# Performance work log

Measured on AMD Instinct MI355X. Metric: run time of the kernel, lower is better.

The kernel has to match this reference:

```python
import jax, jax.numpy as jnp
import numpy as np

INPUT_DIM, K, L, D_C = 512, 3, 512, 64
LN_EPS = 1e-5
NORM_EPS = 1e-12


def setup_inputs() -> dict:
    key = jax.random.key(0)
    ks = jax.random.split(key, 16)
    s = 0.02
    inp = {
        "x": jax.random.normal(ks[0], (65536, INPUT_DIM), jnp.float32),
        # per-sub-encoder MLP weights, stacked over K
        "W1": jax.random.normal(ks[1], (K, INPUT_DIM, 256), jnp.float32) * s,
        "b1": jnp.zeros((K, 256), jnp.float32),
        "W2": jax.random.normal(ks[2], (K, 256, 128), jnp.float32) * s,
        "b2": jnp.zeros((K, 128), jnp.float32),
        "W3": jax.random.normal(ks[3], (K, 128, D_C), jnp.float32) * s,
        "b3": jnp.zeros((K, D_C), jnp.float32),
        # shared output LayerNorm
        "gamma": jnp.ones((D_C,), jnp.float32),
        "beta": jnp.zeros((D_C,), jnp.float32),
        # codebooks: nn.Parameter(torch.randn(L, d_c)) per sub-quantizer
        "codebooks": jax.random.normal(ks[4], (K, L, D_C), jnp.float32),
        # decoder MLP d_c -> 128 -> 256 -> input_dim
        "D1": jax.random.normal(ks[5], (D_C, 128), jnp.float32) * s,
        "c1": jnp.zeros((128,), jnp.float32),
        "D2": jax.random.normal(ks[6], (128, 256), jnp.float32) * s,
        "c2": jnp.zeros((256,), jnp.float32),
        "D3": jax.random.normal(ks[7], (256, INPUT_DIM), jnp.float32) * s,
        "c3": jnp.zeros((INPUT_DIM,), jnp.float32),
    }
    return inp


def _l2norm(v, axis=-1):
    # F.normalize(p=2): x / max(||x||, eps)
    n = jnp.sqrt(jnp.sum(v * v, axis=axis, keepdims=True))
    return v / jnp.maximum(n, NORM_EPS)


def reference(x, W1, b1, W2, b2, W3, b3, gamma, beta, codebooks,
              D1, c1, D2, c2, D3, c3):
    sg = jax.lax.stop_gradient
    # encode all K sub-encoders in one batched einsum: (K, B, *)
    h = jax.nn.relu(jnp.einsum('bi,kio->kbo', x, W1) + b1[:, None, :])
    h = jax.nn.relu(jnp.einsum('kbo,kop->kbp', h, W2) + b2[:, None, :])
    enc = jnp.einsum('kbp,kpd->kbd', h, W3) + b3[:, None, :]  # (K,B,d_c)
    # LayerNorm over d_c
    mu = jnp.mean(enc, axis=-1, keepdims=True)
    var = jnp.mean((enc - mu) ** 2, axis=-1, keepdims=True)
    enc = (enc - mu) * jax.lax.rsqrt(var + LN_EPS) * gamma + beta
    # cosine quantize
    enc_n = _l2norm(enc)
    cb_n = _l2norm(codebooks)                       # (K,L,d_c)
    cos = jnp.einsum('kbd,kld->kbl', enc_n, cb_n)   # (K,B,L)
    idx = jnp.argmax(cos, axis=-1)                  # argmin(1-cos) == argmax(cos), (K,B)
    q = jnp.take_along_axis(cb_n, idx[:, :, None], axis=1)  # (K,B,d_c)
    # straight-through
    q_ste = enc + sg(q - enc)
    codebook_loss = jnp.sum(jnp.mean((sg(enc) - q_ste) ** 2, axis=(1, 2)))
    commitment_loss = jnp.sum(jnp.mean((enc - sg(q_ste)) ** 2, axis=(1, 2)))
    avg_q = jnp.mean(q_ste, axis=0)                 # (B,d_c)
    h = jax.nn.relu(avg_q @ D1 + c1)
    h = jax.nn.relu(h @ D2 + c2)
    reconstructed = h @ D3 + c3                     # (B,input_dim)
    recon_loss = jnp.mean((reconstructed - x) ** 2)
    tokens = idx.T                                  # (B,K)
    return tokens, reconstructed, recon_loss, codebook_loss, commitment_loss
```

## Files before the change

### kernel.cpp

```cpp
#include <hip/hip_runtime.h>

using f4 = float4;

constexpr int IN_DIM = 512;
constexpr int DC     = 64;
constexpr int LCB    = 512;

__device__ __forceinline__ float wave_sum64(float v) {
#pragma unroll
    for (int m = 1; m < 64; m <<= 1) v += __shfl_xor(v, m, 64);
    return v;
}

__global__ void cbnorm_kernel(const float* __restrict__ cb, float* __restrict__ cbn,
                              float* __restrict__ cbnT, float* __restrict__ accv) {
    int row  = blockIdx.x * 4 + (threadIdx.x >> 6);
    int lane = threadIdx.x & 63;
    float v  = cb[(size_t)row * DC + lane];
    float ss = wave_sum64(v * v);
    float n  = sqrtf(ss);
    float o  = v / fmaxf(n, 1e-12f);
    cbn[(size_t)row * DC + lane] = o;
    int k = row >> 9, l = row & 511;
    cbnT[((size_t)k * DC + lane) * LCB + l] = o;
    if (blockIdx.x == 0 && threadIdx.x < 16) accv[threadIdx.x] = 0.f;
}

template <int RELU, int SUM3>
__global__ __launch_bounds__(256, 4)
void gemm_kernel(const float* __restrict__ A, const float* __restrict__ W,
                 const float* __restrict__ bias, float* __restrict__ C,
                 int Kin, int N, float ascale,
                 size_t aK, size_t wK, size_t bK, size_t cK, size_t sumStride) {
    constexpr int BM = 128, BK = 32;
    __shared__ alignas(16) float As[BK][BM + 4];
    __shared__ alignas(16) float Ws[BK][128 + 4];
    const int z = blockIdx.z;
    A += (size_t)z * aK;  W += (size_t)z * wK;
    bias += (size_t)z * bK;  C += (size_t)z * cK;
    const int tid = threadIdx.x;
    const int tx = tid & 15, ty = tid >> 4;
    const int row0 = blockIdx.x * BM, col0 = blockIdx.y * 128;

    float acc[8][8];
#pragma unroll
    for (int i = 0; i < 8; i++)
#pragma unroll
        for (int j = 0; j < 8; j++) acc[i][j] = 0.f;

    const int aRow = tid >> 3;
    const int aCol = (tid & 7) * 4;
    const int wRow = tid >> 5;
    const int wCol = (tid & 31) * 4;

    for (int kk = 0; kk < Kin; kk += BK) {
#pragma unroll
        for (int it = 0; it < 4; it++) {
            const size_t aoff = (size_t)(row0 + aRow + it * 32) * Kin + kk + aCol;
            f4 v = *(const f4*)&A[aoff];
            if (SUM3) {
                f4 v2 = *(const f4*)&A[aoff + sumStride];
                f4 v3 = *(const f4*)&A[aoff + 2 * sumStride];
                v.x += v2.x + v3.x; v.y += v2.y + v3.y;
                v.z += v2.z + v3.z; v.w += v2.w + v3.w;
            }
            As[aCol + 0][aRow + it * 32] = v.x * ascale;
            As[aCol + 1][aRow + it * 32] = v.y * ascale;
            As[aCol + 2][aRow + it * 32] = v.z * ascale;
            As[aCol + 3][aRow + it * 32] = v.w * ascale;
        }
#pragma unroll
        for (int it = 0; it < 4; it++) {
            f4 v = *(const f4*)&W[(size_t)(kk + wRow + it * 8) * N + col0 + wCol];
            *(f4*)&Ws[wRow + it * 8][wCol] = v;
        }
        __syncthreads();
#pragma unroll
        for (int p = 0; p < BK; p++) {
            f4 a0 = *(const f4*)&As[p][ty * 8];
            f4 a1 = *(const f4*)&As[p][ty * 8 + 4];
            f4 w0 = *(const f4*)&Ws[p][tx * 8];
            f4 w1 = *(const f4*)&Ws[p][tx * 8 + 4];
            float av[8] = {a0.x, a0.y, a0.z, a0.w, a1.x, a1.y, a1.z, a1.w};
            float wv[8] = {w0.x, w0.y, w0.z, w0.w, w1.x, w1.y, w1.z, w1.w};
#pragma unroll
            for (int i = 0; i < 8; i++)
#pragma unroll
                for (int j = 0; j < 8; j++)
                    acc[i][j] = fmaf(av[i], wv[j], acc[i][j]);
        }
        __syncthreads();
    }

#pragma unroll
    for (int i = 0; i < 8; i++) {
        const size_t r = (size_t)row0 + ty * 8 + i;
        float vrow[8];
#pragma unroll
        for (int j = 0; j < 8; j++) {
            float v = acc[i][j] + bias[col0 + tx * 8 + j];
            if (RELU) v = fmaxf(v, 0.f);
            vrow[j] = v;
        }
        *(f4*)&C[r * N + col0 + tx * 8]     = *(f4*)&vrow[0];
        *(f4*)&C[r * N + col0 + tx * 8 + 4] = *(f4*)&vrow[4];
    }
}

__global__ __launch_bounds__(256, 4)
void gemm_ln_kernel(const float* __restrict__ A, const float* __restrict__ W,
                    const float* __restrict__ bias, const float* __restrict__ gamma,
                    const float* __restrict__ beta, float* __restrict__ enc, int Kin,
                    size_t aK, size_t wK, size_t bK, size_t eK) {
    constexpr int BM = 128, BK = 32;
    __shared__ alignas(16) float As[BK][BM + 4];
    __shared__ alignas(16) float Ws[BK][DC + 4];
    const int z = blockIdx.y;
    A += (size_t)z * aK;  W += (size_t)z * wK;
    bias += (size_t)z * bK;  enc += (size_t)z * eK;
    const int tid = threadIdx.x;
    const int tx = tid & 7, ty = tid >> 3;
    const int row0 = blockIdx.x * BM;

    float acc[4][8];
#pragma unroll
    for (int i = 0; i < 4; i++)
#pragma unroll
        for (int j = 0; j < 8; j++) acc[i][j] = 0.f;

    const int aRow = tid >> 3;
    const int aCol = (tid & 7) * 4;
    const int wRow = tid >> 4;
    const int wCol = (tid & 15) * 4;

    for (int kk = 0; kk < Kin; kk += BK) {
#pragma unroll
        for (int it = 0; it < 4; it++) {
            f4 v = *(const f4*)&A[(size_t)(row0 + aRow + it * 32) * Kin + kk + aCol];
            As[aCol + 0][aRow + it * 32] = v.x;
            As[aCol + 1][aRow + it * 32] = v.y;
            As[aCol + 2][aRow + it * 32] = v.z;
            As[aCol + 3][aRow + it * 32] = v.w;
        }
#pragma unroll
        for (int it = 0; it < 2; it++) {
            f4 v = *(const f4*)&W[(size_t)(kk + wRow + it * 16) * DC + wCol];
            *(f4*)&Ws[wRow + it * 16][wCol] = v;
        }
        __syncthreads();
#pragma unroll
        for (int p = 0; p < BK; p++) {
            f4 a  = *(const f4*)&As[p][ty * 4];
            f4 w0 = *(const f4*)&Ws[p][tx * 8];
            f4 w1 = *(const f4*)&Ws[p][tx * 8 + 4];
            float av[4] = {a.x, a.y, a.z, a.w};
            float wv[8] = {w0.x, w0.y, w0.z, w0.w, w1.x, w1.y, w1.z, w1.w};
#pragma unroll
            for (int i = 0; i < 4; i++)
#pragma unroll
                for (int j = 0; j < 8; j++)
                    acc[i][j] = fmaf(av[i], wv[j], acc[i][j]);
        }
        __syncthreads();
    }

#pragma unroll
    for (int i = 0; i < 4; i++) {
        float vrow[8];
#pragma unroll
        for (int j = 0; j < 8; j++) vrow[j] = acc[i][j] + bias[tx * 8 + j];
        float s = 0.f;
#pragma unroll
        for (int j = 0; j < 8; j++) s += vrow[j];
#pragma unroll
        for (int m = 1; m < 8; m <<= 1) s += __shfl_xor(s, m, 8);
        float mu = s * (1.f / 64.f);
        float d2 = 0.f;
#pragma unroll
        for (int j = 0; j < 8; j++) { float d = vrow[j] - mu; d2 = fmaf(d, d, d2); }
#pragma unroll
        for (int m = 1; m < 8; m <<= 1) d2 += __shfl_xor(d2, m, 8);
        float rs = 1.f / sqrtf(d2 * (1.f / 64.f) + 1e-5f);
#pragma unroll
        for (int j = 0; j < 8; j++) {
            int c = tx * 8 + j;
            vrow[j] = (vrow[j] - mu) * rs * gamma[c] + beta[c];
        }
        const size_t r = (size_t)row0 + ty * 4 + i;
        *(f4*)&enc[r * DC + tx * 8]     = *(f4*)&vrow[0];
        *(f4*)&enc[r * DC + tx * 8 + 4] = *(f4*)&vrow[4];
    }
}

__global__ __launch_bounds__(256, 2)
void quant_kernel(float* __restrict__ enc, const float* __restrict__ cbT,
                  const float* __restrict__ cbn, float* __restrict__ out_tok,
                  float* __restrict__ sse_acc, int row_off_glob,
                  size_t eK, size_t cbTK, size_t cbnK) {
    constexpr int BM = 128;
    __shared__ alignas(16) float Es[DC][BM + 4];
    __shared__ alignas(16) float Cs[DC][64 + 4];
    __shared__ float red[4];
    const int k = blockIdx.y;
    enc += (size_t)k * eK;
    cbT += (size_t)k * cbTK;
    cbn += (size_t)k * cbnK;
    const int tid = threadIdx.x;
    const int tx = tid & 7, ty = tid >> 3;
    const int row0 = blockIdx.x * BM;

    {
        const int r  = tid >> 1;
        const int c0 = (tid & 1) * 32;
#pragma unroll
        for (int i = 0; i < 8; i++) {
            f4 v = *(const f4*)&enc[(size_t)(row0 + r) * DC + c0 + i * 4];
            Es[c0 + i * 4 + 0][r] = v.x;
            Es[c0 + i * 4 + 1][r] = v.y;
            Es[c0 + i * 4 + 2][r] = v.z;
            Es[c0 + i * 4 + 3][r] = v.w;
        }
    }

    double mx[4]; int mi[4];
#pragma unroll
    for (int i = 0; i < 4; i++) { mx[i] = -1.0e300; mi[i] = 0; }

    for (int lc = 0; lc < LCB; lc += 64) {
        __syncthreads();
        {
            const int p  = tid >> 2;
            const int c0 = (tid & 3) * 16;
#pragma unroll
            for (int i = 0; i < 4; i++)
                *(f4*)&Cs[p][c0 + i * 4] =
                    *(const f4*)&cbT[(size_t)p * LCB + lc + c0 + i * 4];
        }
        __syncthreads();
        double sc[4][8];
#pragma unroll
        for (int i = 0; i < 4; i++)
#pragma unroll
            for (int j = 0; j < 8; j++) sc[i][j] = 0.0;
#pragma unroll
        for (int p = 0; p < DC; p++) {
            f4 a  = *(const f4*)&Es[p][ty * 4];
            f4 w0 = *(const f4*)&Cs[p][tx * 8];
            f4 w1 = *(const f4*)&Cs[p][tx * 8 + 4];
            double av[4] = {a.x, a.y, a.z, a.w};
            double wv[8] = {w0.x, w0.y, w0.z, w0.w, w1.x, w1.y, w1.z, w1.w};
#pragma unroll
            for (int i = 0; i < 4; i++)
#pragma unroll
                for (int j = 0; j < 8; j++)
                    sc[i][j] = fma(av[i], wv[j], sc[i][j]);
        }
#pragma unroll
        for (int i = 0; i < 4; i++)
#pragma unroll
            for (int j = 0; j < 8; j++) {
                int l = lc + tx * 8 + j;
                if (sc[i][j] > mx[i]) { mx[i] = sc[i][j]; mi[i] = l; }
            }
    }

#pragma unroll
    for (int m = 1; m < 8; m <<= 1)
#pragma unroll
        for (int i = 0; i < 4; i++) {
            double omx = __shfl_xor(mx[i], m, 8);
            int    omi = __shfl_xor(mi[i], m, 8);
            if (omx > mx[i] || (omx == mx[i] && omi < mi[i])) { mx[i] = omx; mi[i] = omi; }
        }

    float sse = 0.f;
#pragma unroll
    for (int i = 0; i < 4; i++) {
        const int rl = ty * 4 + i;
        const size_t r = (size_t)row0 + rl;
        f4 q0 = *(const f4*)&cbn[(size_t)mi[i] * DC + tx * 8];
        f4 q1 = *(const f4*)&cbn[(size_t)mi[i] * DC + tx * 8 + 4];
        float qv[8] = {q0.x, q0.y, q0.z, q0.w, q1.x, q1.y, q1.z, q1.w};
#pragma unroll
        for (int j = 0; j < 8; j++) {
            float e = Es[tx * 8 + j][rl];
            float d = e - qv[j];
            sse = fmaf(d, d, sse);
        }
        *(f4*)&enc[r * DC + tx * 8]     = q0;
        *(f4*)&enc[r * DC + tx * 8 + 4] = q1;
        if (tx == 0) out_tok[(size_t)(row_off_glob + r) * 3 + k] = (float)mi[i];
    }
    sse = wave_sum64(sse);
    if ((tid & 63) == 0) red[tid >> 6] = sse;
    __syncthreads();
    if (tid == 0) atomicAdd(sse_acc, red[0] + red[1] + red[2] + red[3]);
}

__global__ __launch_bounds__(256, 4)
void gemm_dec_out_kernel(const float* __restrict__ A, const float* __restrict__ W,
                         const float* __restrict__ bias, const float* __restrict__ x,
                         float* __restrict__ rec, float* __restrict__ sse_acc,
                         int Kin, int N) {
    constexpr int BM = 128, BN = 128, BK = 32;
    __shared__ alignas(16) float As[BK][BM + 4];
    __shared__ alignas(16) float Ws[BK][BN + 4];
    __shared__ float red[4];
    const int tid = threadIdx.x;
    const int tx = tid & 15, ty = tid >> 4;
    const int row0 = blockIdx.x * BM, col0 = blockIdx.y * BN;

    float acc[8][8];
#pragma unroll
    for (int i = 0; i < 8; i++)
#pragma unroll
        for (int j = 0; j < 8; j++) acc[i][j] = 0.f;

    const int aRow = tid >> 3;
    const int aCol = (tid & 7) * 4;
    const int wRow = tid >> 5;
    const int wCol = (tid & 31) * 4;

    for (int kk = 0; kk < Kin; kk += BK) {
#pragma unroll
        for (int it = 0; it < 4; it++) {
            f4 v = *(const f4*)&A[(size_t)(row0 + aRow + it * 32) * Kin + kk + aCol];
            As[aCol + 0][aRow + it * 32] = v.x;
            As[aCol + 1][aRow + it * 32] = v.y;
            As[aCol + 2][aRow + it * 32] = v.z;
            As[aCol + 3][aRow + it * 32] = v.w;
        }
#pragma unroll
        for (int it = 0; it < 4; it++) {
            f4 v = *(const f4*)&W[(size_t)(kk + wRow + it * 8) * N + col0 + wCol];
            *(f4*)&Ws[wRow + it * 8][wCol] = v;
        }
        __syncthreads();
#pragma unroll
        for (int p = 0; p < BK; p++) {
            f4 a0 = *(const f4*)&As[p][ty * 8];
            f4 a1 = *(const f4*)&As[p][ty * 8 + 4];
            f4 w0 = *(const f4*)&Ws[p][tx * 8];
            f4 w1 = *(const f4*)&Ws[p][tx * 8 + 4];
            float av[8] = {a0.x, a0.y, a0.z, a0.w, a1.x, a1.y, a1.z, a1.w};
            float wv[8] = {w0.x, w0.y, w0.z, w0.w, w1.x, w1.y, w1.z, w1.w};
#pragma unroll
            for (int i = 0; i < 8; i++)
#pragma unroll
                for (int j = 0; j < 8; j++)
                    acc[i][j] = fmaf(av[i], wv[j], acc[i][j]);
        }
        __syncthreads();
    }

    float sse = 0.f;
#pragma unroll
    for (int i = 0; i < 8; i++) {
        const size_t r = (size_t)row0 + ty * 8 + i;
        f4 x0 = *(const f4*)&x[r * N + col0 + tx * 8];
        f4 x1 = *(const f4*)&x[r * N + col0 + tx * 8 + 4];
        float xv[8] = {x0.x, x0.y, x0.z, x0.w, x1.x, x1.y, x1.z, x1.w};
        float vrow[8];
#pragma unroll
        for (int j = 0; j < 8; j++) {
            float v = acc[i][j] + bias[col0 + tx * 8 + j];
            float d = v - xv[j];
            sse = fmaf(d, d, sse);
            vrow[j] = v;
        }
        *(f4*)&rec[r * N + col0 + tx * 8]     = *(f4*)&vrow[0];
        *(f4*)&rec[r * N + col0 + tx * 8 + 4] = *(f4*)&vrow[4];
    }
    sse = wave_sum64(sse);
    if ((tid & 63) == 0) red[tid >> 6] = sse;
    __syncthreads();
    if (tid == 0) atomicAdd(sse_acc, red[0] + red[1] + red[2] + red[3]);
}

__global__ void finalize_kernel(const float* __restrict__ accv,
                                float* __restrict__ outs,
                                float inv_rec, float inv_cb) {
    if (threadIdx.x == 0) {
        outs[0] = accv[1] * inv_rec;
        float cbl = accv[0] * inv_cb;
        outs[1] = cbl;
        outs[2] = cbl;
    }
}

extern "C" void kernel_launch(void* const* d_in, const int* in_sizes, int n_in,
                              void* d_out, int out_size, void* d_ws, size_t ws_size,
                              hipStream_t stream) {
    const float* x     = (const float*)d_in[0];
    const float* W1    = (const float*)d_in[1];
    const float* b1    = (const float*)d_in[2];
    const float* W2    = (const float*)d_in[3];
    const float* b2    = (const float*)d_in[4];
    const float* W3    = (const float*)d_in[5];
    const float* b3    = (const float*)d_in[6];
    const float* gamma = (const float*)d_in[7];
    const float* beta  = (const float*)d_in[8];
    const float* cb    = (const float*)d_in[9];
    const float* D1    = (const float*)d_in[10];
    const float* c1    = (const float*)d_in[11];
    const float* D2    = (const float*)d_in[12];
    const float* c2    = (const float*)d_in[13];
    const float* D3    = (const float*)d_in[14];
    const float* c3    = (const float*)d_in[15];
    const int M = in_sizes[0] / IN_DIM;

    float* out     = (float*)d_out;
    float* out_tok = out;
    float* out_rec = out + (size_t)M * 3;
    float* out_sc  = out_rec + (size_t)M * IN_DIM;

    const size_t fixedB  = (size_t)(16 + 2 * 3 * LCB * DC) * 4;
    const size_t perRowB = (size_t)(3 * DC + 3 * 256 + 3 * 128) * 4;
    int C = 4096;
    for (int cand = 65536; cand >= 4096; cand >>= 1)
        if (fixedB + (size_t)cand * perRowB <= ws_size) { C = cand; break; }

    float* ws    = (float*)d_ws;
    float* accv  = ws;
    float* cbn   = accv + 16;
    float* cbnT  = cbn + 3 * LCB * DC;
    float* enc3  = cbnT + 3 * DC * LCB;
    float* H1    = enc3 + (size_t)3 * C * DC;
    float* H2    = H1 + (size_t)3 * C * 256;

    cbnorm_kernel<<<dim3(3 * LCB / 4), dim3(256), 0, stream>>>(cb, cbn, cbnT, accv);

    for (int off = 0; off < M; off += C) {
        const float* xc  = x + (size_t)off * IN_DIM;
        float*       rcc = out_rec + (size_t)off * IN_DIM;

        gemm_kernel<1, 0><<<dim3(C / 128, 2, 3), dim3(256), 0, stream>>>(
            xc, W1, b1, H1, 512, 256, 1.f,
            0, (size_t)512 * 256, 256, (size_t)C * 256, 0);
        gemm_kernel<1, 0><<<dim3(C / 128, 1, 3), dim3(256), 0, stream>>>(
            H1, W2, b2, H2, 256, 128, 1.f,
            (size_t)C * 256, (size_t)256 * 128, 128, (size_t)C * 128, 0);
        gemm_ln_kernel<<<dim3(C / 128, 3), dim3(256), 0, stream>>>(
            H2, W3, b3, gamma, beta, enc3, 128,
            (size_t)C * 128, (size_t)128 * 64, 64, (size_t)C * DC);
        quant_kernel<<<dim3(C / 128, 3), dim3(256), 0, stream>>>(
            enc3, cbnT, cbn, out_tok, accv + 0, off,
            (size_t)C * DC, (size_t)DC * LCB, (size_t)LCB * DC);

        gemm_kernel<1, 1><<<dim3(C / 128, 1, 1), dim3(256), 0, stream>>>(
            enc3, D1, c1, H2, 64, 128, 1.f / 3.f,
            0, 0, 0, 0, (size_t)C * DC);
        gemm_kernel<1, 0><<<dim3(C / 128, 2, 1), dim3(256), 0, stream>>>(
            H2, D2, c2, H1, 128, 256, 1.f, 0, 0, 0, 0, 0);
        gemm_dec_out_kernel<<<dim3(C / 128, 4), dim3(256), 0, stream>>>(
            H1, D3, c3, xc, rcc, accv + 1, 256, 512);
    }

    finalize_kernel<<<dim3(1), dim3(64), 0, stream>>>(
        accv, out_sc, 1.f / ((float)M * IN_DIM), 1.f / ((float)M * DC));
}
```

Measured before the change: 1.374 ms.

## Register-prefetch next K tile in GEMMs and remap LDS layout to cut conflicts

The three tiled GEMM kernels (generic, LN-fused, decoder-output) now load the next K-slice of A and W into registers while the current slice is being computed from shared memory. This overlaps global-memory latency with FMA work, and the loop is rearranged to use a sync before and after the shared-memory store. The transposed A tile padding changes from +4 to +1, which targets bank conflicts on the scattered stores. The W tile drops its padding, and each thread's columns are remapped to tx*4 and 64+tx*4 so shared-memory reads are contiguous across threads, with the epilogue indexing adjusted to match. The +1 row stride makes the float4 reads of As misaligned on odd rows, which may force split or slower LDS accesses, and the extra live registers may reduce occupancy.

```diff
diff --git a/kernel.cpp b/kernel.cpp
--- a/kernel.cpp
+++ b/kernel.cpp
@@ -32,15 +32,15 @@
                  const float* __restrict__ bias, float* __restrict__ C,
                  int Kin, int N, float ascale,
                  size_t aK, size_t wK, size_t bK, size_t cK, size_t sumStride) {
-    constexpr int BM = 128, BK = 32;
-    __shared__ alignas(16) float As[BK][BM + 4];
-    __shared__ alignas(16) float Ws[BK][128 + 4];
+    constexpr int BM = 128, BN = 128, BK = 32;
+    __shared__ alignas(16) float As[BK][BM + 1];
+    __shared__ alignas(16) float Ws[BK][BN];
     const int z = blockIdx.z;
     A += (size_t)z * aK;  W += (size_t)z * wK;
     bias += (size_t)z * bK;  C += (size_t)z * cK;
     const int tid = threadIdx.x;
     const int tx = tid & 15, ty = tid >> 4;
-    const int row0 = blockIdx.x * BM, col0 = blockIdx.y * 128;
+    const int row0 = blockIdx.x * BM, col0 = blockIdx.y * BN;
 
     float acc[8][8];
 #pragma unroll
@@ -53,34 +53,52 @@
     const int wRow = tid >> 5;
     const int wCol = (tid & 31) * 4;
 
+    f4 ra[4], rw[4];
+#pragma unroll
+    for (int it = 0; it < 4; it++) {
+        const size_t aoff = (size_t)(row0 + aRow + it * 32) * Kin + aCol;
+        ra[it] = *(const f4*)&A[aoff];
+        if (SUM3) {
+            f4 v2 = *(const f4*)&A[aoff + sumStride];
+            f4 v3 = *(const f4*)&A[aoff + 2 * sumStride];
+            ra[it].x += v2.x + v3.x; ra[it].y += v2.y + v3.y;
+            ra[it].z += v2.z + v3.z; ra[it].w += v2.w + v3.w;
+        }
+        rw[it] = *(const f4*)&W[(size_t)(wRow + it * 8) * N + col0 + wCol];
+    }
+
     for (int kk = 0; kk < Kin; kk += BK) {
+        __syncthreads();
 #pragma unroll
         for (int it = 0; it < 4; it++) {
-            const size_t aoff = (size_t)(row0 + aRow + it * 32) * Kin + kk + aCol;
-            f4 v = *(const f4*)&A[aoff];
-            if (SUM3) {
-                f4 v2 = *(const f4*)&A[aoff + sumStride];
-                f4 v3 = *(const f4*)&A[aoff + 2 * sumStride];
-                v.x += v2.x + v3.x; v.y += v2.y + v3.y;
-                v.z += v2.z + v3.z; v.w += v2.w + v3.w;
+            As[aCol + 0][aRow + it * 32] = ra[it].x * ascale;
+            As[aCol + 1][aRow + it * 32] = ra[it].y * ascale;
+            As[aCol + 2][aRow + it * 32] = ra[it].z * ascale;
+            As[aCol + 3][aRow + it * 32] = ra[it].w * ascale;
+            *(f4*)&Ws[wRow + it * 8][wCol] = rw[it];
+        }
+        __syncthreads();
+        if (kk + BK < Kin) {
+            const int kn = kk + BK;
+#pragma unroll
+            for (int it = 0; it < 4; it++) {
+                const size_t aoff = (size_t)(row0 + aRow + it * 32) * Kin + kn + aCol;
+                ra[it] = *(const f4*)&A[aoff];
+                if (SUM3) {
+                    f4 v2 = *(const f4*)&A[aoff + sumStride];
+                    f4 v3 = *(const f4*)&A[aoff + 2 * sumStride];
+                    ra[it].x += v2.x + v3.x; ra[it].y += v2.y + v3.y;
+                    ra[it].z += v2.z + v3.z; ra[it].w += v2.w + v3.w;
+                }
+                rw[it] = *(const f4*)&W[(size_t)(kn + wRow + it * 8) * N + col0 + wCol];
             }
-            As[aCol + 0][aRow + it * 32] = v.x * ascale;
-            As[aCol + 1][aRow + it * 32] = v.y * ascale;
-            As[aCol + 2][aRow + it * 32] = v.z * ascale;
-            As[aCol + 3][aRow + it * 32] = v.w * ascale;
-        }
-#pragma unroll
-        for (int it = 0; it < 4; it++) {
-            f4 v = *(const f4*)&W[(size_t)(kk + wRow + it * 8) * N + col0 + wCol];
-            *(f4*)&Ws[wRow + it * 8][wCol] = v;
-        }
-        __syncthreads();
+        }
 #pragma unroll
         for (int p = 0; p < BK; p++) {
             f4 a0 = *(const f4*)&As[p][ty * 8];
             f4 a1 = *(const f4*)&As[p][ty * 8 + 4];
-            f4 w0 = *(const f4*)&Ws[p][tx * 8];
-            f4 w1 = *(const f4*)&Ws[p][tx * 8 + 4];
+            f4 w0 = *(const f4*)&Ws[p][tx * 4];
+            f4 w1 = *(const f4*)&Ws[p][64 + tx * 4];
             float av[8] = {a0.x, a0.y, a0.z, a0.w, a1.x, a1.y, a1.z, a1.w};
             float wv[8] = {w0.x, w0.y, w0.z, w0.w, w1.x, w1.y, w1.z, w1.w};
 #pragma unroll
@@ -89,7 +107,6 @@
                 for (int j = 0; j < 8; j++)
                     acc[i][j] = fmaf(av[i], wv[j], acc[i][j]);
         }
-        __syncthreads();
     }
 
 #pragma unroll
@@ -97,13 +114,19 @@
         const size_t r = (size_t)row0 + ty * 8 + i;
         float vrow[8];
 #pragma unroll
-        for (int j = 0; j < 8; j++) {
-            float v = acc[i][j] + bias[col0 + tx * 8 + j];
+        for (int j = 0; j < 4; j++) {
+            float v = acc[i][j] + bias[col0 + tx * 4 + j];
             if (RELU) v = fmaxf(v, 0.f);
             vrow[j] = v;
         }
-        *(f4*)&C[r * N + col0 + tx * 8]     = *(f4*)&vrow[0];
-        *(f4*)&C[r * N + col0 + tx * 8 + 4] = *(f4*)&vrow[4];
+#pragma unroll
+        for (int j = 4; j < 8; j++) {
+            float v = acc[i][j] + bias[col0 + 64 + tx * 4 + j - 4];
+            if (RELU) v = fmaxf(v, 0.f);
+            vrow[j] = v;
+        }
+        *(f4*)&C[r * N + col0 + tx * 4]      = *(f4*)&vrow[0];
+        *(f4*)&C[r * N + col0 + 64 + tx * 4] = *(f4*)&vrow[4];
     }
 }
 
@@ -113,7 +136,7 @@
                     const float* __restrict__ beta, float* __restrict__ enc, int Kin,
                     size_t aK, size_t wK, size_t bK, size_t eK) {
     constexpr int BM = 128, BK = 32;
-    __shared__ alignas(16) float As[BK][BM + 4];
+    __shared__ alignas(16) float As[BK][BM + 1];
     __shared__ alignas(16) float Ws[BK][DC + 4];
     const int z = blockIdx.y;
     A += (size_t)z * aK;  W += (size_t)z * wK;
@@ -133,21 +156,36 @@
     const int wRow = tid >> 4;
     const int wCol = (tid & 15) * 4;
 
+    f4 ra[4], rw[2];
+#pragma unroll
+    for (int it = 0; it < 4; it++)
+        ra[it] = *(const f4*)&A[(size_t)(row0 + aRow + it * 32) * Kin + aCol];
+#pragma unroll
+    for (int it = 0; it < 2; it++)
+        rw[it] = *(const f4*)&W[(size_t)(wRow + it * 16) * DC + wCol];
+
     for (int kk = 0; kk < Kin; kk += BK) {
+        __syncthreads();
 #pragma unroll
         for (int it = 0; it < 4; it++) {
-            f4 v = *(const f4*)&A[(size_t)(row0 + aRow + it * 32) * Kin + kk + aCol];
-            As[aCol + 0][aRow + it * 32] = v.x;
-            As[aCol + 1][aRow + it * 32] = v.y;
-            As[aCol + 2][aRow + it * 32] = v.z;
-            As[aCol + 3][aRow + it * 32] = v.w;
-        }
-#pragma unroll
-        for (int it = 0; it < 2; it++) {
-            f4 v = *(const f4*)&W[(size_t)(kk + wRow + it * 16) * DC + wCol];
-            *(f4*)&Ws[wRow + it * 16][wCol] = v;
-        }
-        __syncthreads();
+            As[aCol + 0][aRow + it * 32] = ra[it].x;
+            As[aCol + 1][aRow + it * 32] = ra[it].y;
+            As[aCol + 2][aRow + it * 32] = ra[it].z;
+            As[aCol + 3][aRow + it * 32] = ra[it].w;
+        }
+#pragma unroll
+        for (int it = 0; it < 2; it++)
+            *(f4*)&Ws[wRow + it * 16][wCol] = rw[it];
+        __syncthreads();
+        if (kk + BK < Kin) {
+            const int kn = kk + BK;
+#pragma unroll
+            for (int it = 0; it < 4; it++)
+                ra[it] = *(const f4*)&A[(size_t)(row0 + aRow + it * 32) * Kin + kn + aCol];
+#pragma unroll
+            for (int it = 0; it < 2; it++)
+                rw[it] = *(const f4*)&W[(size_t)(kn + wRow + it * 16) * DC + wCol];
+        }
 #pragma unroll
         for (int p = 0; p < BK; p++) {
             f4 a  = *(const f4*)&As[p][ty * 4];
@@ -161,7 +199,6 @@
                 for (int j = 0; j < 8; j++)
                     acc[i][j] = fmaf(av[i], wv[j], acc[i][j]);
         }
-        __syncthreads();
     }
 
 #pragma unroll
@@ -303,8 +340,8 @@
                          float* __restrict__ rec, float* __restrict__ sse_acc,
                          int Kin, int N) {
     constexpr int BM = 128, BN = 128, BK = 32;
-    __shared__ alignas(16) float As[BK][BM + 4];
-    __shared__ alignas(16) float Ws[BK][BN + 4];
+    __shared__ alignas(16) float As[BK][BM + 1];
+    __shared__ alignas(16) float Ws[BK][BN];
     __shared__ float red[4];
     const int tid = threadIdx.x;
     const int tx = tid & 15, ty = tid >> 4;
@@ -321,27 +358,38 @@
     const int wRow = tid >> 5;
     const int wCol = (tid & 31) * 4;
 
+    f4 ra[4], rw[4];
+#pragma unroll
+    for (int it = 0; it < 4; it++) {
+        ra[it] = *(const f4*)&A[(size_t)(row0 + aRow + it * 32) * Kin + aCol];
+        rw[it] = *(const f4*)&W[(size_t)(wRow + it * 8) * N + col0 + wCol];
+    }
+
     for (int kk = 0; kk < Kin; kk += BK) {
+        __syncthreads();
 #pragma unroll
         for (int it = 0; it < 4; it++) {
-            f4 v = *(const f4*)&A[(size_t)(row0 + aRow + it * 32) * Kin + kk + aCol];
-            As[aCol + 0][aRow + it * 32] = v.x;
-            As[aCol + 1][aRow + it * 32] = v.y;
-            As[aCol + 2][aRow + it * 32] = v.z;
-            As[aCol + 3][aRow + it * 32] = v.w;
-        }
-#pragma unroll
-        for (int it = 0; it < 4; it++) {
-            f4 v = *(const f4*)&W[(size_t)(kk + wRow + it * 8) * N + col0 + wCol];
-            *(f4*)&Ws[wRow + it * 8][wCol] = v;
-        }
-        __syncthreads();
+            As[aCol + 0][aRow + it * 32] = ra[it].x;
+            As[aCol + 1][aRow + it * 32] = ra[it].y;
+            As[aCol + 2][aRow + it * 32] = ra[it].z;
+            As[aCol + 3][aRow + it * 32] = ra[it].w;
+            *(f4*)&Ws[wRow + it * 8][wCol] = rw[it];
+        }
+        __syncthreads();
+        if (kk + BK < Kin) {
+            const int kn = kk + BK;
+#pragma unroll
+            for (int it = 0; it < 4; it++) {
+                ra[it] = *(const f4*)&A[(size_t)(row0 + aRow + it * 32) * Kin + kn + aCol];
+                rw[it] = *(const f4*)&W[(size_t)(kn + wRow + it * 8) * N + col0 + wCol];
+            }
+        }
 #pragma unroll
         for (int p = 0; p < BK; p++) {
             f4 a0 = *(const f4*)&As[p][ty * 8];
             f4 a1 = *(const f4*)&As[p][ty * 8 + 4];
-            f4 w0 = *(const f4*)&Ws[p][tx * 8];
-            f4 w1 = *(const f4*)&Ws[p][tx * 8 + 4];
+            f4 w0 = *(const f4*)&Ws[p][tx * 4];
+            f4 w1 = *(const f4*)&Ws[p][64 + tx * 4];
             float av[8] = {a0.x, a0.y, a0.z, a0.w, a1.x, a1.y, a1.z, a1.w};
             float wv[8] = {w0.x, w0.y, w0.z, w0.w, w1.x, w1.y, w1.z, w1.w};
 #pragma unroll
@@ -350,26 +398,32 @@
                 for (int j = 0; j < 8; j++)
                     acc[i][j] = fmaf(av[i], wv[j], acc[i][j]);
         }
-        __syncthreads();
     }
 
     float sse = 0.f;
 #pragma unroll
     for (int i = 0; i < 8; i++) {
         const size_t r = (size_t)row0 + ty * 8 + i;
-        f4 x0 = *(const f4*)&x[r * N + col0 + tx * 8];
-        f4 x1 = *(const f4*)&x[r * N + col0 + tx * 8 + 4];
+        f4 x0 = *(const f4*)&x[r * N + col0 + tx * 4];
+        f4 x1 = *(const f4*)&x[r * N + col0 + 64 + tx * 4];
         float xv[8] = {x0.x, x0.y, x0.z, x0.w, x1.x, x1.y, x1.z, x1.w};
         float vrow[8];
 #pragma unroll
-        for (int j = 0; j < 8; j++) {
-            float v = acc[i][j] + bias[col0 + tx * 8 + j];
+        for (int j = 0; j < 4; j++) {
+            float v = acc[i][j] + bias[col0 + tx * 4 + j];
             float d = v - xv[j];
             sse = fmaf(d, d, sse);
             vrow[j] = v;
         }
-        *(f4*)&rec[r * N + col0 + tx * 8]     = *(f4*)&vrow[0];
-        *(f4*)&rec[r * N + col0 + tx * 8 + 4] = *(f4*)&vrow[4];
+#pragma unroll
+        for (int j = 4; j < 8; j++) {
+            float v = acc[i][j] + bias[col0 + 64 + tx * 4 + j - 4];
+            float d = v - xv[j];
+            sse = fmaf(d, d, sse);
+            vrow[j] = v;
+        }
+        *(f4*)&rec[r * N + col0 + tx * 4]      = *(f4*)&vrow[0];
+        *(f4*)&rec[r * N + col0 + 64 + tx * 4] = *(f4*)&vrow[4];
     }
     sse = wave_sum64(sse);
     if ((tid & 63) == 0) red[tid >> 6] = sse;
```

Measured after the change: 2.474 ms. 80.0% more time.
